# Kernel optimization log

Hardware: AMD Instinct MI355X
Metric: run time of the kernel (lower is better)

Reference implementation:

```python
import jax, jax.numpy as jnp
import numpy as np

D_MODEL = 768
NUM_HEADS = 12
HEAD_DIM = D_MODEL // NUM_HEADS


def setup_inputs() -> dict:
    key = jax.random.key(0)
    ks = jax.random.split(key, 9)
    B, S = 2, 2048
    s = 1.0 / np.sqrt(D_MODEL)
    x = jax.random.normal(ks[0], (B, S, D_MODEL), dtype=jnp.float32)
    Wq = jax.random.normal(ks[1], (D_MODEL, D_MODEL), dtype=jnp.float32) * s
    Wk = jax.random.normal(ks[2], (D_MODEL, D_MODEL), dtype=jnp.float32) * s
    Wv = jax.random.normal(ks[3], (D_MODEL, D_MODEL), dtype=jnp.float32) * s
    Wo = jax.random.normal(ks[4], (D_MODEL, D_MODEL), dtype=jnp.float32) * s
    bq = jax.random.normal(ks[5], (D_MODEL,), dtype=jnp.float32) * 0.01
    bk = jax.random.normal(ks[6], (D_MODEL,), dtype=jnp.float32) * 0.01
    bv = jax.random.normal(ks[7], (D_MODEL,), dtype=jnp.float32) * 0.01
    bo = jax.random.normal(ks[8], (D_MODEL,), dtype=jnp.float32) * 0.01
    return {"x": x, "Wq": Wq, "bq": bq, "Wk": Wk, "bk": bk,
            "Wv": Wv, "bv": bv, "Wo": Wo, "bo": bo}


def reference(x, Wq, bq, Wk, bk, Wv, bv, Wo, bo):
    B, S, _ = x.shape
    # projections; reshape to [B, H, S, Dh]
    def split_heads(t):
        return t.reshape(B, S, NUM_HEADS, HEAD_DIM).transpose(0, 2, 1, 3)
    q = split_heads(x @ Wq + bq)
    k = split_heads(x @ Wk + bk)
    v = split_heads(x @ Wv + bv)
    scale = 1.0 / np.sqrt(HEAD_DIM)
    scores = jnp.einsum("bhqd,bhkd->bhqk", q, k) * scale  # [B,H,S,S]
    attn = jax.nn.softmax(scores, axis=-1)
    # dropout p=0.0 (eval) -> identity
    ctx = jnp.einsum("bhqk,bhkd->bhqd", attn, v)
    ctx = ctx.transpose(0, 2, 1, 3).reshape(B, S, D_MODEL)
    return ctx @ Wo + bo
```

## Files before the change

kernel.cpp:

```cpp
#include <hip/hip_runtime.h>
#include <hip/hip_bf16.h>
#include <hip/hip_fp16.h>

#define D_MODEL 768
#define NHEADS  12
#define HD      64
#define BATCH   2
#define SEQ     2048
#define NTOK    (BATCH*SEQ)
#define NX      ((size_t)NTOK * D_MODEL)
#define NW      ((size_t)D_MODEL * D_MODEL)
#define NBH     (BATCH*NHEADS)
#define SC_LOG2 0.18033688f

typedef __attribute__((ext_vector_type(8))) short    short8;
typedef __attribute__((ext_vector_type(8))) _Float16 half8;
typedef __attribute__((ext_vector_type(2))) __fp16   fp16x2;
typedef __attribute__((ext_vector_type(4))) float    f32x4;

__device__ __forceinline__ float bf2f(short s) {
    union { unsigned u; float f; } c;
    c.u = ((unsigned)(unsigned short)s) << 16;
    return c.f;
}
__device__ __forceinline__ short f2bf(float f) {
    __hip_bfloat16 h = __float2bfloat16(f);
    return *(short*)&h;
}

#ifdef __has_builtin
#if __has_builtin(__builtin_amdgcn_global_load_lds)
#define HAS_GLD 1
#endif
#if __has_builtin(__builtin_amdgcn_exp2f)
#define EXP2(x) __builtin_amdgcn_exp2f(x)
#else
#define EXP2(x) exp2f(x)
#endif
#if __has_builtin(__builtin_amdgcn_cvt_pkrtz)
#define HAS_PKRTZ 1
#endif
#else
#define EXP2(x) exp2f(x)
#endif
#ifdef HAS_GLD
#define GLD16(gp, lp) __builtin_amdgcn_global_load_lds( \
    (const __attribute__((address_space(1))) void*)(gp), \
    (__attribute__((address_space(3))) void*)(lp), 16, 0, 0)
#endif

#ifdef HAS_PKRTZ
#define PKF16(a, b) __builtin_amdgcn_cvt_pkrtz((a), (b))
#else
#define PKF16(a, b) ((fp16x2){ (__fp16)(a), (__fp16)(b) })
#endif

__global__ __launch_bounds__(256) void fused_conv(
        const void* __restrict__ xin,
        const void* __restrict__ w0, const void* __restrict__ w1,
        const void* __restrict__ w2, const void* __restrict__ w3,
        const void* __restrict__ b0, const void* __restrict__ b1,
        const void* __restrict__ b2, const void* __restrict__ b3,
        short* __restrict__ xc, short* __restrict__ wt,
        short* __restrict__ bc, int* __restrict__ flag)
{
    __shared__ int red[256];
    __shared__ float T[64][65];
    const int tid = threadIdx.x;
    const int F = blockIdx.x;

    {
        const short* xs = (const short*)xin;
        int maxe = 0;
#pragma unroll
        for (int u = 0; u < 16; ++u) {
            int e = ((unsigned short)xs[tid * 16 + u] >> 7) & 0xFF;
            maxe = max(maxe, e);
        }
        red[tid] = maxe;
        __syncthreads();
        for (int s = 128; s > 0; s >>= 1) {
            if (tid < s) red[tid] = max(red[tid], red[tid + s]);
            __syncthreads();
        }
    }
    const bool isf = (red[0] > 140);

    if (F < 3072) {
        const int i = F * 256 + tid;
        if (isf) {
            float4 f = ((const float4*)xin)[i];
            short4 o = { f2bf(f.x), f2bf(f.y), f2bf(f.z), f2bf(f.w) };
            ((short4*)xc)[i] = o;
        } else {
            ((short4*)xc)[i] = ((const short4*)xin)[i];
        }
    } else if (F < 3648) {
        const int G = F - 3072;
        const int z = G / 144, rr = G % 144;
        const int k0 = (rr % 12) * 64, n0 = (rr / 12) * 64;
        const void* src = (z == 0) ? w0 : (z == 1) ? w1 : (z == 2) ? w2 : w3;
        const float sc = (z == 0) ? SC_LOG2 : 1.0f;
        const int la = tid & 15, lb = tid >> 4;
#pragma unroll
        for (int u = 0; u < 4; ++u) {
            const int kr = (lb & 3) + 4 * u + 16 * (lb >> 2);
            if (isf) {
                float4 f = *(const float4*)((const float*)src + (size_t)(k0 + kr) * D_MODEL + n0 + la * 4);
                T[kr][la*4+0] = f.x; T[kr][la*4+1] = f.y; T[kr][la*4+2] = f.z; T[kr][la*4+3] = f.w;
            } else {
                short4 s = *(const short4*)((const short*)src + (size_t)(k0 + kr) * D_MODEL + n0 + la * 4);
                T[kr][la*4+0] = bf2f(s.x); T[kr][la*4+1] = bf2f(s.y);
                T[kr][la*4+2] = bf2f(s.z); T[kr][la*4+3] = bf2f(s.w);
            }
        }
        __syncthreads();
#pragma unroll
        for (int u = 0; u < 4; ++u) {
            const int nr = (lb & 3) + 4 * u + 16 * (lb >> 2);
            short4 o = { f2bf(T[la*4+0][nr] * sc), f2bf(T[la*4+1][nr] * sc),
                         f2bf(T[la*4+2][nr] * sc), f2bf(T[la*4+3][nr] * sc) };
            *(short4*)(wt + (size_t)z * NW + (size_t)(n0 + nr) * D_MODEL + k0 + la * 4) = o;
        }
    } else {
        if (tid == 0) *flag = isf ? 1 : 0;
        const void* srcs[4] = { b0, b1, b2, b3 };
        for (int z = 0; z < 4; ++z) {
            const float sc = (z == 0) ? SC_LOG2 : 1.0f;
            for (int i = tid; i < D_MODEL; i += 256) {
                float v = isf ? ((const float*)srcs[z])[i] : bf2f(((const short*)srcs[z])[i]);
                bc[z * D_MODEL + i] = f2bf(v * sc);
            }
        }
    }
}

__global__ __launch_bounds__(256) void qkv_gemm(const short* __restrict__ X,
                                                const short* __restrict__ Wt,
                                                const short* __restrict__ bias,
                                                short* __restrict__ qb,
                                                short* __restrict__ kb,
                                                _Float16* __restrict__ Vt)
{
    __shared__ __align__(16) char shbuf[24576];
    short* Als = (short*)shbuf;
    short* Bls = (short*)(shbuf + 8192);
    _Float16* T = (_Float16*)shbuf;

    const int tid = threadIdx.x;
    const int wave = tid >> 6, lane = tid & 63;
    const int quad = lane >> 4, l16 = lane & 15;
    const int wm = wave & 1, wn = wave >> 1;
    const int m0 = blockIdx.x * 64;
    const int ng = blockIdx.y * 128;

    f32x4 acc[2][4];
#pragma unroll
    for (int nt = 0; nt < 4; ++nt) {
        const float bv = bf2f(bias[ng + wn*64 + nt*16 + l16]);
#pragma unroll
        for (int mt = 0; mt < 2; ++mt) acc[mt][nt] = (f32x4){bv, bv, bv, bv};
    }

    const int row = tid >> 2, ch = (tid & 3) * 8;
#ifdef HAS_GLD
#define QSTAGE(buf, k0) do { \
        GLD16(X  + (size_t)(m0 + row)      * D_MODEL + (k0) + ch, &Als[(buf)*2048 + tid*8]); \
        GLD16(Wt + (size_t)(ng + row)      * D_MODEL + (k0) + ch, &Bls[(buf)*4096 + tid*8]); \
        GLD16(Wt + (size_t)(ng + 64 + row) * D_MODEL + (k0) + ch, &Bls[(buf)*4096 + 2048 + tid*8]); \
    } while (0)
#else
#define QSTAGE(buf, k0) do { \
        short8 r0 = *(const short8*)(X  + (size_t)(m0 + row)      * D_MODEL + (k0) + ch); \
        short8 r2 = *(const short8*)(Wt + (size_t)(ng + row)      * D_MODEL + (k0) + ch); \
        short8 r3 = *(const short8*)(Wt + (size_t)(ng + 64 + row) * D_MODEL + (k0) + ch); \
        *(short8*)&Als[(buf)*2048 + tid*8] = r0; \
        *(short8*)&Bls[(buf)*4096 + tid*8] = r2; \
        *(short8*)&Bls[(buf)*4096 + 2048 + tid*8] = r3; \
    } while (0)
#endif

    QSTAGE(0, 0);
    __syncthreads();

    for (int ks = 0; ks < 24; ++ks) {
        const int cur = ks & 1;
        if (ks + 1 < 24) QSTAGE(cur ^ 1, (ks + 1) * 32);

        short8 a[2], b[4];
#pragma unroll
        for (int mt = 0; mt < 2; ++mt)
            a[mt] = *(const short8*)&Als[cur*2048 + (wm*32 + mt*16 + l16) * 32 + quad*8];
#pragma unroll
        for (int nt = 0; nt < 4; ++nt)
            b[nt] = *(const short8*)&Bls[cur*4096 + (wn*64 + nt*16 + l16) * 32 + quad*8];
#pragma unroll
        for (int mt = 0; mt < 2; ++mt)
#pragma unroll
        for (int nt = 0; nt < 4; ++nt)
            acc[mt][nt] = __builtin_amdgcn_mfma_f32_16x16x32_bf16(a[mt], b[nt], acc[mt][nt], 0, 0, 0);

        __syncthreads();
    }
#undef QSTAGE

    const int seg = blockIdx.y / 6;
    if (seg < 2) {
        short* out = seg ? kb : qb;
        const int nl = ng - seg * 768;
#pragma unroll
        for (int mt = 0; mt < 2; ++mt)
#pragma unroll
        for (int nt = 0; nt < 4; ++nt) {
            const int n = nl + wn*64 + nt*16 + l16;
#pragma unroll
            for (int r = 0; r < 4; ++r) {
                const int m = m0 + wm*32 + mt*16 + quad*4 + r;
                out[(size_t)m * D_MODEL + n] = f2bf(acc[mt][nt][r]);
            }
        }
    } else {
        const int batch = m0 >> 11, tokb = m0 & (SEQ - 1);
#pragma unroll
        for (int nt = 0; nt < 4; ++nt) {
            const int dim_l = wn*64 + nt*16 + l16;
#pragma unroll
            for (int mt = 0; mt < 2; ++mt) {
                const int tok_l = wm*32 + mt*16 + quad*4;
                union { _Float16 h4[4]; int2 v; } u;
#pragma unroll
                for (int r = 0; r < 4; ++r) u.h4[r] = (_Float16)acc[mt][nt][r];
                *(int2*)&T[dim_l * 72 + tok_l] = u.v;
            }
        }
        __syncthreads();
#pragma unroll
        for (int u = 0; u < 4; ++u) {
            const int slot = tid + u * 256;
            const int drow = slot >> 3, chk = slot & 7;
            int4 val = *(const int4*)&T[drow * 72 + chk * 8];
            const int dim_g = ng - 1536 + drow;
            const int h = dim_g >> 6, d = dim_g & 63;
            *(int4*)(Vt + ((size_t)(batch * NHEADS + h) * HD + d) * SEQ + tokb + chk*8) = val;
        }
    }
}

__global__ __launch_bounds__(256) void out_gemm(const short* __restrict__ X,
                                                const short* __restrict__ Wt,
                                                const short* __restrict__ bias,
                                                void* __restrict__ outv,
                                                const int* __restrict__ flag)
{
    __shared__ short Als[2][2048];
    __shared__ short Bls[2][2048];

    const int tid = threadIdx.x;
    const int wave = tid >> 6, lane = tid & 63;
    const int quad = lane >> 4, l16 = lane & 15;
    const int m0 = blockIdx.x * 64;
    const int n0 = blockIdx.y * 64;

    f32x4 acc[4];
#pragma unroll
    for (int nt = 0; nt < 4; ++nt) {
        const float bv = bf2f(bias[n0 + nt*16 + l16]);
        acc[nt] = (f32x4){bv, bv, bv, bv};
    }

    const int row = tid >> 2, ch = (tid & 3) * 8;
#ifdef HAS_GLD
#define OSTAGE(buf, k0) do { \
        GLD16(X  + (size_t)(m0 + row) * D_MODEL + (k0) + ch, &Als[buf][tid*8]); \
        GLD16(Wt + (size_t)(n0 + row) * D_MODEL + (k0) + ch, &Bls[buf][tid*8]); \
    } while (0)
#else
#define OSTAGE(buf, k0) do { \
        short8 r0 = *(const short8*)(X  + (size_t)(m0 + row) * D_MODEL + (k0) + ch); \
        short8 r1 = *(const short8*)(Wt + (size_t)(n0 + row) * D_MODEL + (k0) + ch); \
        *(short8*)&Als[buf][tid*8] = r0; \
        *(short8*)&Bls[buf][tid*8] = r1; \
    } while (0)
#endif

    OSTAGE(0, 0);
    __syncthreads();

    for (int ks = 0; ks < 24; ++ks) {
        const int cur = ks & 1;
        if (ks + 1 < 24) OSTAGE(cur ^ 1, (ks + 1) * 32);

        short8 a = *(const short8*)&Als[cur][(wave*16 + l16) * 32 + quad*8];
#pragma unroll
        for (int nt = 0; nt < 4; ++nt) {
            short8 b = *(const short8*)&Bls[cur][(nt*16 + l16) * 32 + quad*8];
            acc[nt] = __builtin_amdgcn_mfma_f32_16x16x32_bf16(a, b, acc[nt], 0, 0, 0);
        }
        __syncthreads();
    }
#undef OSTAGE

    const bool outf32 = (*flag != 0);
#pragma unroll
    for (int nt = 0; nt < 4; ++nt) {
        const int n = n0 + nt*16 + l16;
#pragma unroll
        for (int r = 0; r < 4; ++r) {
            const int m = m0 + wave*16 + quad*4 + r;
            const size_t idx = (size_t)m * D_MODEL + n;
            if (outf32) ((float*)outv)[idx] = acc[nt][r];
            else        ((short*)outv)[idx] = f2bf(acc[nt][r]);
        }
    }
}

__global__ __launch_bounds__(256, 3) void attn_mfma(const short* __restrict__ q,
                                                    const short* __restrict__ k,
                                                    const _Float16* __restrict__ Vt,
                                                    _Float16* __restrict__ Op,
                                                    float* __restrict__ mlp)
{
    __shared__ __align__(16) short    Kls[2][4096];
    __shared__ __align__(16) _Float16 Vls[2][4096];
    __shared__ __align__(16) _Float16 Pls[4][2048];

    const int tid  = threadIdx.x;
    const int wave = tid >> 6, lane = tid & 63;
    const int quad = lane >> 4, l16 = lane & 15;

    const int F = blockIdx.x;
    const int xcd = F & 7, slot = F >> 3;
    const int bh = xcd * 3 + (slot >> 5);
    const int rem = slot & 31;
    const int q0 = (rem >> 1) * 128;
    const int sp = rem & 1;
    const int kb0 = sp * (SEQ / 2);
    const int b = bh / NHEADS, h = bh % NHEADS;
    const size_t bS = (size_t)b * SEQ;

    short8 qf[2][2];
#pragma unroll
    for (int col = 0; col < 2; ++col)
#pragma unroll
    for (int k0h = 0; k0h < 2; ++k0h)
        qf[col][k0h] = *(const short8*)(q + (bS + q0 + wave*32 + col*16 + l16) * D_MODEL
                                          + h*HD + k0h*32 + quad*8);

    half8 ones;
#pragma unroll
    for (int j = 0; j < 8; ++j) ones[j] = (_Float16)1.0f;

    const int cK0 = tid >> 6,         keyK0 = tid & 63;
    const int cK1 = (tid + 256) >> 6, keyK1 = tid & 63;
    const short* kgp0 = k + (bS + kb0 + keyK0) * D_MODEL + h*HD + cK0*8;
    const short* kgp1 = k + (bS + kb0 + keyK1) * D_MODEL + h*HD + cK1*8;
    const _Float16* vgp0 = Vt + ((size_t)bh * HD + keyK0) * SEQ + kb0 + cK0*8;
    const _Float16* vgp1 = Vt + ((size_t)bh * HD + keyK1) * SEQ + kb0 + cK1*8;

#ifdef HAS_GLD
#define STAGE_K(buf, j0) do { \
        GLD16(kgp0 + (size_t)(j0) * D_MODEL, &Kls[buf][tid*8]); \
        GLD16(kgp1 + (size_t)(j0) * D_MODEL, &Kls[buf][(tid+256)*8]); \
    } while (0)
#define STAGE_V(buf, j0) do { \
        GLD16(vgp0 + (j0), &Vls[buf][tid*8]); \
        GLD16(vgp1 + (j0), &Vls[buf][(tid+256)*8]); \
    } while (0)
#else
#define STAGE_K(buf, j0) do { \
        short8 a_ = *(const short8*)(kgp0 + (size_t)(j0) * D_MODEL); \
        short8 b_ = *(const short8*)(kgp1 + (size_t)(j0) * D_MODEL); \
        *(short8*)&Kls[buf][tid*8] = a_;  *(short8*)&Kls[buf][(tid+256)*8] = b_; \
    } while (0)
#define STAGE_V(buf, j0) do { \
        half8 c_ = *(const half8*)(vgp0 + (j0)); \
        half8 d_ = *(const half8*)(vgp1 + (j0)); \
        *(half8*)&Vls[buf][tid*8] = c_;  *(half8*)&Vls[buf][(tid+256)*8] = d_; \
    } while (0)
#endif

    float m_ = -1e30f;
    f32x4 laccA = (f32x4){0.f,0.f,0.f,0.f}, laccB = (f32x4){0.f,0.f,0.f,0.f};
    f32x4 o[4][2];
#pragma unroll
    for (int t = 0; t < 4; ++t) { o[t][0] = (f32x4){0.f,0.f,0.f,0.f}; o[t][1] = (f32x4){0.f,0.f,0.f,0.f}; }

#define NT (SEQ / 2 / 64)

#define QK(S, KB) do { \
    _Pragma("unroll") \
    for (int t = 0; t < 4; ++t) { S[t][0] = (f32x4){0.f,0.f,0.f,0.f}; S[t][1] = (f32x4){0.f,0.f,0.f,0.f}; } \
    _Pragma("unroll") \
    for (int k0h = 0; k0h < 2; ++k0h) \
    _Pragma("unroll") \
    for (int t = 0; t < 4; ++t) { \
        short8 kf = *(const short8*)&Kls[KB][(k0h*4 + quad)*512 + (t*16 + l16)*8]; \
        S[t][0] = __builtin_amdgcn_mfma_f32_16x16x32_bf16(kf, qf[0][k0h], S[t][0], 0, 0, 0); \
        S[t][1] = __builtin_amdgcn_mfma_f32_16x16x32_bf16(kf, qf[1][k0h], S[t][1], 0, 0, 0); \
    } \
} while (0)

#define PV(VB) do { \
    _Pragma("unroll") \
    for (int k0h = 0; k0h < 2; ++k0h) { \
        half8 pf0 = *(half8*)&Pls[wave][(k0h*4 + quad)*128 + l16*8]; \
        half8 pf1 = *(half8*)&Pls[wave][1024 + (k0h*4 + quad)*128 + l16*8]; \
        laccA = __builtin_amdgcn_mfma_f32_16x16x32_f16(ones, pf0, laccA, 0, 0, 0); \
        laccB = __builtin_amdgcn_mfma_f32_16x16x32_f16(ones, pf1, laccB, 0, 0, 0); \
        _Pragma("unroll") \
        for (int t = 0; t < 4; ++t) { \
            half8 vf = *(const half8*)&Vls[VB][(k0h*4 + quad)*512 + (t*16 + l16)*8]; \
            o[t][0] = __builtin_amdgcn_mfma_f32_16x16x32_f16(vf, pf0, o[t][0], 0, 0, 0); \
            o[t][1] = __builtin_amdgcn_mfma_f32_16x16x32_f16(vf, pf1, o[t][1], 0, 0, 0); \
        } \
    } \
} while (0)

#define SOFTMAX(S) do { \
    float mx = S[0][0][0]; \
    _Pragma("unroll") \
    for (int t = 0; t < 4; ++t) \
    _Pragma("unroll") \
    for (int c = 0; c < 2; ++c) \
    _Pragma("unroll") \
    for (int r = 0; r < 4; ++r) mx = fmaxf(mx, S[t][c][r]); \
    if (__any(mx > m_ + 8.f)) { \
        _Pragma("unroll") \
        for (int d = 1; d < 64; d <<= 1) mx = fmaxf(mx, __shfl_xor(mx, d)); \
        const float mn = fmaxf(m_, mx); \
        const float al = EXP2(m_ - mn); \
        _Pragma("unroll") \
        for (int t = 0; t < 4; ++t) \
        _Pragma("unroll") \
        for (int c = 0; c < 2; ++c) { \
            o[t][c][0] *= al; o[t][c][1] *= al; o[t][c][2] *= al; o[t][c][3] *= al; \
        } \
        laccA[0] *= al; laccB[0] *= al; \
        m_ = mn; \
    } \
    _Pragma("unroll") \
    for (int t = 0; t < 4; ++t) \
    _Pragma("unroll") \
    for (int c = 0; c < 2; ++c) { \
        union { fp16x2 h2[2]; int2 v; } u4; \
        u4.h2[0] = PKF16(EXP2(S[t][c][0] - m_), EXP2(S[t][c][1] - m_)); \
        u4.h2[1] = PKF16(EXP2(S[t][c][2] - m_), EXP2(S[t][c][3] - m_)); \
        const int kc = 2*t + (quad >> 1); \
        *(int2*)&Pls[wave][c*1024 + kc*128 + l16*8 + (quad & 1)*4] = u4.v; \
    } \
} while (0)

#define BODY(JT) do { \
    if ((JT) + 2 < NT) STAGE_K(((JT) + 2) & 1, ((JT) + 2) * 64); \
    if ((JT) + 1 < NT) STAGE_V(((JT) + 1) & 1, ((JT) + 1) * 64); \
    f32x4 s_[4][2]; \
    __builtin_amdgcn_s_setprio(1); \
    if ((JT) + 1 < NT) QK(s_, ((JT) + 1) & 1); \
    PV((JT) & 1); \
    __builtin_amdgcn_s_setprio(0); \
    if ((JT) + 1 < NT) SOFTMAX(s_); \
    __syncthreads(); \
} while (0)

    STAGE_K(0, 0); STAGE_V(0, 0);
    __syncthreads();
    STAGE_K(1, 64);
    {
        f32x4 s_[4][2];
        QK(s_, 0);
        SOFTMAX(s_);
    }
    __syncthreads();

    for (int jt = 0; jt < NT; ++jt) BODY(jt);

#pragma unroll
    for (int col = 0; col < 2; ++col) {
        const f32x4 la = col ? laccB : laccA;
        const float inv = 1.0f / la[0];
        const int myq = q0 + wave*32 + col*16 + l16;
        const size_t prow = ((size_t)sp * (NBH * SEQ) + (size_t)bh * SEQ + myq);
        _Float16* orow = Op + prow * HD;
#pragma unroll
        for (int t = 0; t < 4; ++t) {
            union { _Float16 h4[4]; int2 v; } u4;
#pragma unroll
            for (int r = 0; r < 4; ++r) u4.h4[r] = (_Float16)(o[t][col][r] * inv);
            *(int2*)(orow + t*16 + quad*4) = u4.v;
        }
        if (quad == 0) {
            float2 mlv; mlv.x = m_; mlv.y = la[0];
            *(float2*)&mlp[prow * 2] = mlv;
        }
    }
#undef BODY
#undef SOFTMAX
#undef PV
#undef QK
#undef NT
#undef STAGE_K
#undef STAGE_V
}

__global__ __launch_bounds__(256) void attn_combine(const _Float16* __restrict__ Op,
                                                    const float* __restrict__ mlp,
                                                    short* __restrict__ ctx)
{
    const int gid = blockIdx.x * 256 + threadIdx.x;
    const int r = gid >> 3, seg = gid & 7;
    const float2 a  = *(const float2*)&mlp[(size_t)r * 2];
    const float2 c2 = *(const float2*)&mlp[((size_t)(NBH * SEQ) + r) * 2];
    const float M  = fmaxf(a.x, c2.x);
    const float w1 = EXP2(a.x - M) * a.y;
    const float w2 = EXP2(c2.x - M) * c2.y;
    const float inv = 1.0f / (w1 + w2);
    const half8 o1 = *(const half8*)&Op[(size_t)r * HD + seg * 8];
    const half8 o2 = *(const half8*)&Op[(size_t)(NBH * SEQ) * HD + (size_t)r * HD + seg * 8];
    union { short s[8]; int4 v; } u;
#pragma unroll
    for (int j = 0; j < 8; ++j)
        u.s[j] = f2bf((w1 * (float)o1[j] + w2 * (float)o2[j]) * inv);
    const int bh = r >> 11, qq = r & (SEQ - 1);
    const int bb = bh / NHEADS, hh = bh % NHEADS;
    *(int4*)&ctx[((size_t)(bb * SEQ + qq)) * D_MODEL + hh * HD + seg * 8] = u.v;
}

extern "C" void kernel_launch(void* const* d_in, const int* in_sizes, int n_in,
                              void* d_out, int out_size, void* d_ws, size_t ws_size,
                              hipStream_t stream)
{
    int* flag = (int*)d_ws;
    short* xc = (short*)((char*)d_ws + 64);
    short* Wt = xc + NX;
    short* bc = Wt + 4 * NW;
    short* qb = bc + 4 * D_MODEL;
    short* kb = qb + NX;
    _Float16* Vt = (_Float16*)(kb + NX);
    short* cb = (short*)(Vt + NX);
    _Float16* Op = (_Float16*)(cb + NX);
    float* mlp = (float*)(Op + (size_t)2 * NBH * SEQ * HD);

    fused_conv<<<3649, 256, 0, stream>>>(d_in[0],
                                         d_in[1], d_in[3], d_in[5], d_in[7],
                                         d_in[2], d_in[4], d_in[6], d_in[8],
                                         xc, Wt, bc, flag);

    qkv_gemm<<<dim3(NTOK/64, 2304/128), 256, 0, stream>>>(xc, Wt, bc, qb, kb, Vt);

    attn_mfma<<<768, 256, 0, stream>>>(qb, kb, Vt, Op, mlp);

    attn_combine<<<1536, 256, 0, stream>>>(Op, mlp, cb);

    out_gemm<<<dim3(NTOK/64, D_MODEL/64), 256, 0, stream>>>(cb, Wt + 3*NW, bc + 3*D_MODEL, d_out, flag);
}
```

Before: 174.5 us.

## Fuse split-KV attention combine into output projection GEMM A-tile staging

Removes the separate attn_combine kernel and its ctx buffer. The out_gemm now reads both partial attention outputs and their max/sum stats directly while staging the A tile, merges them in registers and writes bf16 into LDS. This saves one launch and a full write and read of the context tensor. In exchange, the combine math is recomputed in each of the 12 N-column blocks, and the A load becomes a synchronous register path instead of an async global-to-LDS copy.

```diff
diff --git a/kernel.cpp b/kernel.cpp
--- a/kernel.cpp
+++ b/kernel.cpp
@@ -246,7 +246,8 @@
     }
 }
 
-__global__ __launch_bounds__(256) void out_gemm(const short* __restrict__ X,
+__global__ __launch_bounds__(256) void out_gemm(const _Float16* __restrict__ Op,
+                                                const float* __restrict__ mlp,
                                                 const short* __restrict__ Wt,
                                                 const short* __restrict__ bias,
                                                 void* __restrict__ outv,
@@ -269,23 +270,43 @@
     }
 
     const int row = tid >> 2, ch = (tid & 3) * 8;
+    const int m = m0 + row;
+    const int bhb = (m >> 11) * NHEADS;
+    const int qq = m & (SEQ - 1);
+
+#define OSTAGE(buf, k0) do { \
+        const int cc = (k0) + ch; \
+        const int h = cc >> 6, d = cc & 63; \
+        const size_t r1 = (size_t)(bhb + h) * SEQ + qq; \
+        const float2 ml1 = *(const float2*)&mlp[r1 * 2]; \
+        const float2 ml2 = *(const float2*)&mlp[((size_t)(NBH * SEQ) + r1) * 2]; \
+        const float M_ = fmaxf(ml1.x, ml2.x); \
+        const float w1 = EXP2(ml1.x - M_) * ml1.y; \
+        const float w2 = EXP2(ml2.x - M_) * ml2.y; \
+        const float s_ = 1.0f / (w1 + w2); \
+        const float f1 = w1 * s_, f2 = w2 * s_; \
+        const half8 o1 = *(const half8*)&Op[r1 * HD + d]; \
+        const half8 o2 = *(const half8*)&Op[(size_t)(NBH * SEQ) * HD + r1 * HD + d]; \
+        short8 xb; \
+        _Pragma("unroll") \
+        for (int j = 0; j < 8; ++j) \
+            xb[j] = f2bf(f1 * (float)o1[j] + f2 * (float)o2[j]); \
+        *(short8*)&Als[buf][tid*8] = xb; \
+        GLD16_OR_REG(buf, k0); \
+    } while (0)
 #ifdef HAS_GLD
-#define OSTAGE(buf, k0) do { \
-        GLD16(X  + (size_t)(m0 + row) * D_MODEL + (k0) + ch, &Als[buf][tid*8]); \
-        GLD16(Wt + (size_t)(n0 + row) * D_MODEL + (k0) + ch, &Bls[buf][tid*8]); \
-    } while (0)
+#define GLD16_OR_REG(buf, k0) \
+        GLD16(Wt + (size_t)(n0 + row) * D_MODEL + (k0) + ch, &Bls[buf][tid*8])
 #else
-#define OSTAGE(buf, k0) do { \
-        short8 r0 = *(const short8*)(X  + (size_t)(m0 + row) * D_MODEL + (k0) + ch); \
-        short8 r1 = *(const short8*)(Wt + (size_t)(n0 + row) * D_MODEL + (k0) + ch); \
-        *(short8*)&Als[buf][tid*8] = r0; \
-        *(short8*)&Bls[buf][tid*8] = r1; \
-    } while (0)
+#define GLD16_OR_REG(buf, k0) do { \
+        short8 r1_ = *(const short8*)(Wt + (size_t)(n0 + row) * D_MODEL + (k0) + ch); \
+        *(short8*)&Bls[buf][tid*8] = r1_; } while (0)
 #endif
 
     OSTAGE(0, 0);
     __syncthreads();
 
+#pragma unroll 2
     for (int ks = 0; ks < 24; ++ks) {
         const int cur = ks & 1;
         if (ks + 1 < 24) OSTAGE(cur ^ 1, (ks + 1) * 32);
@@ -299,6 +320,7 @@
         __syncthreads();
     }
 #undef OSTAGE
+#undef GLD16_OR_REG
 
     const bool outf32 = (*flag != 0);
 #pragma unroll
@@ -306,8 +328,8 @@
         const int n = n0 + nt*16 + l16;
 #pragma unroll
         for (int r = 0; r < 4; ++r) {
-            const int m = m0 + wave*16 + quad*4 + r;
-            const size_t idx = (size_t)m * D_MODEL + n;
+            const int mm = m0 + wave*16 + quad*4 + r;
+            const size_t idx = (size_t)mm * D_MODEL + n;
             if (outf32) ((float*)outv)[idx] = acc[nt][r];
             else        ((short*)outv)[idx] = f2bf(acc[nt][r]);
         }
@@ -502,29 +524,6 @@
 #undef STAGE_V
 }
 
-__global__ __launch_bounds__(256) void attn_combine(const _Float16* __restrict__ Op,
-                                                    const float* __restrict__ mlp,
-                                                    short* __restrict__ ctx)
-{
-    const int gid = blockIdx.x * 256 + threadIdx.x;
-    const int r = gid >> 3, seg = gid & 7;
-    const float2 a  = *(const float2*)&mlp[(size_t)r * 2];
-    const float2 c2 = *(const float2*)&mlp[((size_t)(NBH * SEQ) + r) * 2];
-    const float M  = fmaxf(a.x, c2.x);
-    const float w1 = EXP2(a.x - M) * a.y;
-    const float w2 = EXP2(c2.x - M) * c2.y;
-    const float inv = 1.0f / (w1 + w2);
-    const half8 o1 = *(const half8*)&Op[(size_t)r * HD + seg * 8];
-    const half8 o2 = *(const half8*)&Op[(size_t)(NBH * SEQ) * HD + (size_t)r * HD + seg * 8];
-    union { short s[8]; int4 v; } u;
-#pragma unroll
-    for (int j = 0; j < 8; ++j)
-        u.s[j] = f2bf((w1 * (float)o1[j] + w2 * (float)o2[j]) * inv);
-    const int bh = r >> 11, qq = r & (SEQ - 1);
-    const int bb = bh / NHEADS, hh = bh % NHEADS;
-    *(int4*)&ctx[((size_t)(bb * SEQ + qq)) * D_MODEL + hh * HD + seg * 8] = u.v;
-}
-
 extern "C" void kernel_launch(void* const* d_in, const int* in_sizes, int n_in,
                               void* d_out, int out_size, void* d_ws, size_t ws_size,
                               hipStream_t stream)
@@ -536,8 +535,7 @@
     short* qb = bc + 4 * D_MODEL;
     short* kb = qb + NX;
     _Float16* Vt = (_Float16*)(kb + NX);
-    short* cb = (short*)(Vt + NX);
-    _Float16* Op = (_Float16*)(cb + NX);
+    _Float16* Op = (_Float16*)(Vt + NX);
     float* mlp = (float*)(Op + (size_t)2 * NBH * SEQ * HD);
 
     fused_conv<<<3649, 256, 0, stream>>>(d_in[0],
@@ -549,7 +547,5 @@
 
     attn_mfma<<<768, 256, 0, stream>>>(qb, kb, Vt, Op, mlp);
 
-    attn_combine<<<1536, 256, 0, stream>>>(Op, mlp, cb);
-
-    out_gemm<<<dim3(NTOK/64, D_MODEL/64), 256, 0, stream>>>(cb, Wt + 3*NW, bc + 3*D_MODEL, d_out, flag);
-}
+    out_gemm<<<dim3(NTOK/64, D_MODEL/64), 256, 0, stream>>>(Op, mlp, Wt + 3*NW, bc + 3*D_MODEL, d_out, flag);
+}
```

Measured after the change: 175.4 us. No clear change (+0.5%).
